# Kernel tuning notes

Measured on AMD Instinct MI355X. Metric: run time of the kernel, lower is better.

## Reference

```python
import jax, jax.numpy as jnp
import numpy as np

NEG = -1e9

def setup_inputs() -> dict:
    key = jax.random.key(0)
    k1, k2, k3, k4, k5 = jax.random.split(key, 5)
    B, S, D = 4, 2048, 1024
    x = jax.random.normal(k1, (B, S, D), dtype=jnp.float32)
    Wq = jax.random.normal(k2, (D, D), dtype=jnp.float32) * (1.0 / np.sqrt(D))
    Wk = jax.random.normal(k3, (D, D), dtype=jnp.float32) * (1.0 / np.sqrt(D))
    Wv = jax.random.normal(k4, (D, D), dtype=jnp.float32) * (1.0 / np.sqrt(D))
    mask = jax.random.randint(k5, (B, S), 0, 2) > 0  # bool [B,S]
    return {"x": x, "Wq": Wq, "Wk": Wk, "Wv": Wv, "mask": mask}

def reference(x, Wq, Wk, Wv, mask):
    # x: [B,S,D]; single-head self-attention, scale = 1/sqrt(D)
    D = x.shape[-1]
    scale = 1.0 / D ** 0.5
    q = jnp.einsum('bsi,ij->bsj', x, Wq)
    k = jnp.einsum('bsi,ij->bsj', x, Wk)
    y = jnp.einsum('bsi,bzi->bsz', q, k) * scale  # [B,S,S]
    # additive mask: (~mask)[:, :, None] * -1e9 broadcasts over key axis
    m = (~mask).astype(jnp.float32)[:, :, None]
    y = y + m * NEG
    v = jnp.einsum('bsi,ij->bsj', x, Wv)
    attn = jax.nn.softmax(y, axis=-1)
    return jnp.einsum('bsz,bzi->bsi', attn, v)
```

## Files before the change

kernel.cpp:

```cpp
#include <hip/hip_runtime.h>

typedef __bf16 bf16x8 __attribute__((ext_vector_type(8)));
typedef float f32x4 __attribute__((ext_vector_type(4)));
typedef unsigned short u16;

__device__ __forceinline__ u16 f2bf(float f) {
    union { float f; unsigned u; } v; v.f = f;
    unsigned r = (v.u + 0x7FFFu + ((v.u >> 16) & 1u)) >> 16;
    return (u16)r;
}

__device__ __forceinline__ void fence_bar() {
    asm volatile("" ::: "memory");
    __builtin_amdgcn_s_barrier();
    asm volatile("" ::: "memory");
}

__global__ __launch_bounds__(256)
void normMask(const unsigned int* __restrict__ m, unsigned char* __restrict__ nm) {
    __shared__ int isByte;
    if (threadIdx.x == 0) isByte = 0;
    __syncthreads();
    int bad = 0;
    for (int i = threadIdx.x; i < 2048; i += 256) bad |= (m[i] > 1u);
    if (bad) atomicOr(&isByte, 1);
    __syncthreads();
    if (isByte) {
        const unsigned char* mb = (const unsigned char*)m;
        for (int i = threadIdx.x; i < 8192; i += 256) nm[i] = mb[i] ? 1 : 0;
    } else {
        for (int i = threadIdx.x; i < 8192; i += 256) nm[i] = (unsigned char)m[i];
    }
}

__global__ __launch_bounds__(256)
void transW(const float* __restrict__ Wq, const float* __restrict__ Wk,
            const float* __restrict__ Wv, u16* __restrict__ Wt) {
    __shared__ u16 tile[64][65];
    const float* W = blockIdx.z == 0 ? Wq : (blockIdx.z == 1 ? Wk : Wv);
    u16* out = Wt + (size_t)blockIdx.z * 1024 * 1024;
    int k0 = blockIdx.x * 64, n0 = blockIdx.y * 64;
    int t = threadIdx.x, cl = t & 63, rw = t >> 6;
    #pragma unroll
    for (int r = 0; r < 16; ++r) {
        int row = r * 4 + rw;
        tile[cl][row] = f2bf(W[(size_t)(k0 + row) * 1024 + n0 + cl]);
    }
    __syncthreads();
    #pragma unroll
    for (int r = 0; r < 16; ++r) {
        int row = r * 4 + rw;
        out[(size_t)(n0 + row) * 1024 + k0 + cl] = tile[row][cl];
    }
}

__global__ __launch_bounds__(256)
void convX(const float* __restrict__ x, u16* __restrict__ xb) {
    const size_t n4 = (size_t)8192 * 1024 / 4;
    for (size_t i = (size_t)blockIdx.x * 256 + threadIdx.x; i < n4; i += (size_t)gridDim.x * 256) {
        float4 v = ((const float4*)x)[i];
        ushort4 o = make_ushort4(f2bf(v.x), f2bf(v.y), f2bf(v.z), f2bf(v.w));
        ((ushort4*)xb)[i] = o;
    }
}

__global__ __launch_bounds__(256)
void transV(const u16* __restrict__ qkv, u16* __restrict__ vt) {
    __shared__ u16 tile[64][65];
    int b = blockIdx.z;
    int s0 = blockIdx.x * 64, d0 = blockIdx.y * 64;
    int t = threadIdx.x, cl = t & 63, rw = t >> 6;
    const u16* src = qkv + (size_t)b * 2048 * 3072 + 2048;
    #pragma unroll
    for (int r = 0; r < 16; ++r) {
        int row = r * 4 + rw;
        tile[cl][row] = src[(size_t)(s0 + row) * 3072 + d0 + cl];
    }
    __syncthreads();
    u16* dst = vt + (size_t)b * 1024 * 2048;
    #pragma unroll
    for (int r = 0; r < 16; ++r) {
        int row = r * 4 + rw;
        dst[(size_t)(d0 + row) * 2048 + s0 + cl] = tile[row][cl];
    }
}

template <int OUTV>
__global__ __launch_bounds__(512, 2)
void gemm8p(const u16* __restrict__ A_, int lda, size_t sA,
            const u16* __restrict__ B_, int ldb, size_t sB,
            void* __restrict__ Cout, int ldc, size_t sC,
            int kdim, int ntiles) {
    __shared__ u16 lds[65536];
    const u16* A = A_ + (size_t)blockIdx.z * sA;
    const u16* B = B_ + (size_t)blockIdx.z * sB;

    const int bid = blockIdx.x;
    const int brow = (bid / ntiles) * 256, bcol = (bid % ntiles) * 256;
    const int t = threadIdx.x;
    const int w = t >> 6, l = t & 63;
    const int wr = w >> 2, wc = w & 3;

    const int srow = t >> 3;
    const int sslot = (t & 7) ^ (srow & 7);
    const int aBase = (wr * 128 + (l & 15)) * 64;
    const int bBase = 32768 + (wc * 64 + (l & 15)) * 64;
    const int cx0 = (((l >> 4)) ^ (l & 7)) * 8;
    const int cx1 = (((l >> 4) + 4) ^ (l & 7)) * 8;

    auto lds3 = (__attribute__((address_space(3))) char*)lds;

    #define ISSUE(matB, q, tt, buf) do {                                           \
        const u16* gsrc = ((matB) ? B : A)                                         \
            + (size_t)(((matB) ? bcol : brow) + (q) * 64 + srow) * ((matB) ? ldb : lda) \
            + (size_t)(tt) * 64 + sslot * 8;                                       \
        const int dst_ = ((matB) ? 32768 : 0) + (buf) * 16384 + (q) * 4096 + t * 8; \
        __builtin_amdgcn_global_load_lds(                                          \
            (const __attribute__((address_space(1))) void*)gsrc,                   \
            (__attribute__((address_space(3))) void*)(lds3 + 2 * dst_), 16, 0, 0); \
    } while (0)

    f32x4 acc[8][4];
    #pragma unroll
    for (int m = 0; m < 8; ++m)
        #pragma unroll
        for (int n = 0; n < 4; ++n)
            acc[m][n] = (f32x4){0.f, 0.f, 0.f, 0.f};

    const int NT = kdim >> 6;

    ISSUE(1, 0, 0, 0); ISSUE(1, 1, 0, 0); ISSUE(1, 2, 0, 0); ISSUE(1, 3, 0, 0);
    ISSUE(0, 0, 0, 0); ISSUE(0, 2, 0, 0); ISSUE(0, 1, 0, 0); ISSUE(0, 3, 0, 0);
    asm volatile("s_waitcnt vmcnt(2)" ::: "memory");
    fence_bar();

    for (int tt = 0; tt < NT; ++tt) {
        const int c = tt & 1;
        const int ab = c * 16384;
        const int nb = c ^ 1;
        const bool pf = (tt + 1 < NT);
        bf16x8 af[4], bfv[4];

        #pragma unroll
        for (int m = 0; m < 4; ++m) af[m] = *(const bf16x8*)&lds[ab + aBase + m * 1024 + cx0];
        #pragma unroll
        for (int n = 0; n < 4; ++n) bfv[n] = *(const bf16x8*)&lds[ab + bBase + n * 1024 + cx0];
        if (pf) {
            ISSUE(1, 0, tt + 1, nb); ISSUE(1, 1, tt + 1, nb);
            asm volatile("s_waitcnt vmcnt(2)" ::: "memory");
        } else {
            asm volatile("s_waitcnt vmcnt(0)" ::: "memory");
        }
        fence_bar();
        __builtin_amdgcn_s_setprio(1);
        #pragma unroll
        for (int m = 0; m < 4; ++m)
            #pragma unroll
            for (int n = 0; n < 4; ++n)
                acc[m][n] = __builtin_amdgcn_mfma_f32_16x16x32_bf16(af[m], bfv[n], acc[m][n], 0, 0, 0);
        __builtin_amdgcn_s_setprio(0);
        fence_bar();

        #pragma unroll
        for (int m = 0; m < 4; ++m) af[m] = *(const bf16x8*)&lds[ab + aBase + (m + 4) * 1024 + cx0];
        if (pf) { ISSUE(1, 2, tt + 1, nb); ISSUE(1, 3, tt + 1, nb); }
        fence_bar();
        __builtin_amdgcn_s_setprio(1);
        #pragma unroll
        for (int m = 0; m < 4; ++m)
            #pragma unroll
            for (int n = 0; n < 4; ++n)
                acc[m + 4][n] = __builtin_amdgcn_mfma_f32_16x16x32_bf16(af[m], bfv[n], acc[m + 4][n], 0, 0, 0);
        __builtin_amdgcn_s_setprio(0);
        fence_bar();

        #pragma unroll
        for (int m = 0; m < 4; ++m) af[m] = *(const bf16x8*)&lds[ab + aBase + m * 1024 + cx1];
        #pragma unroll
        for (int n = 0; n < 4; ++n) bfv[n] = *(const bf16x8*)&lds[ab + bBase + n * 1024 + cx1];
        if (pf) { ISSUE(0, 0, tt + 1, nb); ISSUE(0, 2, tt + 1, nb); }
        fence_bar();
        __builtin_amdgcn_s_setprio(1);
        #pragma unroll
        for (int m = 0; m < 4; ++m)
            #pragma unroll
            for (int n = 0; n < 4; ++n)
                acc[m][n] = __builtin_amdgcn_mfma_f32_16x16x32_bf16(af[m], bfv[n], acc[m][n], 0, 0, 0);
        __builtin_amdgcn_s_setprio(0);
        fence_bar();

        #pragma unroll
        for (int m = 0; m < 4; ++m) af[m] = *(const bf16x8*)&lds[ab + aBase + (m + 4) * 1024 + cx1];
        if (pf) {
            ISSUE(0, 1, tt + 1, nb); ISSUE(0, 3, tt + 1, nb);
            asm volatile("s_waitcnt vmcnt(2)" ::: "memory");
        } else {
            asm volatile("s_waitcnt vmcnt(0)" ::: "memory");
        }
        fence_bar();
        __builtin_amdgcn_s_setprio(1);
        #pragma unroll
        for (int m = 0; m < 4; ++m)
            #pragma unroll
            for (int n = 0; n < 4; ++n)
                acc[m + 4][n] = __builtin_amdgcn_mfma_f32_16x16x32_bf16(af[m], bfv[n], acc[m + 4][n], 0, 0, 0);
        __builtin_amdgcn_s_setprio(0);
        fence_bar();
    }
    #undef ISSUE

    const int lr = (l >> 4) * 4, lc = l & 15;
    #pragma unroll
    for (int m = 0; m < 8; ++m) {
        #pragma unroll
        for (int n = 0; n < 4; ++n) {
            int rr = brow + wr * 128 + m * 16 + lr;
            int cc = bcol + wc * 64 + n * 16 + lc;
            #pragma unroll
            for (int j = 0; j < 4; ++j) {
                if constexpr (OUTV == 0)
                    ((u16*)Cout)[(size_t)blockIdx.z * sC + (size_t)(rr + j) * ldc + cc] = f2bf(acc[m][n][j]);
                else
                    ((float*)Cout)[(size_t)blockIdx.z * sC + (size_t)(rr + j) * ldc + cc] = acc[m][n][j];
            }
        }
    }
}

template <int OUTV>
__global__ __launch_bounds__(256, 2)
void gemm_bt(const u16* __restrict__ A0, int lda, size_t sA,
             const u16* __restrict__ B0, int ldb, size_t sB,
             void* __restrict__ Cout, int ldc, size_t sC, int kdim) {
    __shared__ u16 lA[128 * 64];
    __shared__ u16 lB[128 * 64];
    const u16* A = A0 + (size_t)blockIdx.z * sA;
    const u16* B = B0 + (size_t)blockIdx.z * sB;
    const int t = threadIdx.x;
    const int w = t >> 6, l = t & 63;
    const int wr = w >> 1, wc = w & 1;
    const int brow = blockIdx.x * 128, bcol = blockIdx.y * 128;
    const int rt = l >> 3;
    const int cb = (l & 7) * 8;

    auto ldsA3 = (__attribute__((address_space(3))) char*)lA;
    auto ldsB3 = (__attribute__((address_space(3))) char*)lB;

    f32x4 acc[4][4];
    #pragma unroll
    for (int m = 0; m < 4; ++m)
        #pragma unroll
        for (int n = 0; n < 4; ++n)
            acc[m][n] = (f32x4){0.f, 0.f, 0.f, 0.f};

    for (int k0 = 0; k0 < kdim; k0 += 64) {
        __syncthreads();
        #pragma unroll
        for (int p = 0; p < 4; ++p) {
            int chunk = p * 4 + w;
            const u16* ga = A + (size_t)(brow + chunk * 8 + rt) * lda + k0 + cb;
            __builtin_amdgcn_global_load_lds(
                (const __attribute__((address_space(1))) void*)ga,
                (__attribute__((address_space(3))) void*)(ldsA3 + chunk * 1024), 16, 0, 0);
            const u16* gb = B + (size_t)(bcol + chunk * 8 + rt) * ldb + k0 + cb;
            __builtin_amdgcn_global_load_lds(
                (const __attribute__((address_space(1))) void*)gb,
                (__attribute__((address_space(3))) void*)(ldsB3 + chunk * 1024), 16, 0, 0);
        }
        __syncthreads();
        #pragma unroll
        for (int kk = 0; kk < 2; ++kk) {
            bf16x8 af[4], bfv[4];
            #pragma unroll
            for (int m = 0; m < 4; ++m)
                af[m] = *(const bf16x8*)&lA[(wr * 64 + m * 16 + (l & 15)) * 64 + kk * 32 + (l >> 4) * 8];
            #pragma unroll
            for (int n = 0; n < 4; ++n)
                bfv[n] = *(const bf16x8*)&lB[(wc * 64 + n * 16 + (l & 15)) * 64 + kk * 32 + (l >> 4) * 8];
            #pragma unroll
            for (int m = 0; m < 4; ++m)
                #pragma unroll
                for (int n = 0; n < 4; ++n)
                    acc[m][n] = __builtin_amdgcn_mfma_f32_16x16x32_bf16(af[m], bfv[n], acc[m][n], 0, 0, 0);
        }
    }

    const int lrow = (l >> 4) * 4, lcol = l & 15;
    #pragma unroll
    for (int m = 0; m < 4; ++m) {
        #pragma unroll
        for (int n = 0; n < 4; ++n) {
            int rr = brow + wr * 64 + m * 16 + lrow;
            int cc = bcol + wc * 64 + n * 16 + lcol;
            #pragma unroll
            for (int j = 0; j < 4; ++j) {
                if constexpr (OUTV == 0)
                    ((u16*)Cout)[(size_t)blockIdx.z * sC + (size_t)(rr + j) * ldc + cc] = f2bf(acc[m][n][j]);
                else
                    ((float*)Cout)[(size_t)blockIdx.z * sC + (size_t)(rr + j) * ldc + cc] = acc[m][n][j];
            }
        }
    }
}

__global__ __launch_bounds__(256)
void softmax_rows(const float* __restrict__ S0, size_t sS, u16* __restrict__ P0, size_t sP,
                  const unsigned char* __restrict__ nm, int bbase) {
    const int row = blockIdx.x, t = threadIdx.x;
    const int b = bbase + blockIdx.z;
    const float* S = S0 + (size_t)blockIdx.z * sS;
    u16* dst = P0 + (size_t)blockIdx.z * sP + (size_t)row * 2048;
    if (nm[b * 2048 + row] == 0) {
        ushort4 u = make_ushort4(0x3A00, 0x3A00, 0x3A00, 0x3A00);
        ((ushort4*)dst)[t] = u;
        ((ushort4*)dst)[t + 256] = u;
        return;
    }
    const float4* src = (const float4*)(S + (size_t)row * 2048);
    float4 a = src[t], c = src[t + 256];
    float v[8] = {a.x, a.y, a.z, a.w, c.x, c.y, c.z, c.w};
    float mx = -1e30f;
    #pragma unroll
    for (int i = 0; i < 8; ++i) { v[i] *= 0.03125f; mx = fmaxf(mx, v[i]); }
    #pragma unroll
    for (int o = 32; o > 0; o >>= 1) mx = fmaxf(mx, __shfl_xor(mx, o));
    __shared__ float redm[4], reds[4];
    if ((t & 63) == 0) redm[t >> 6] = mx;
    __syncthreads();
    mx = fmaxf(fmaxf(redm[0], redm[1]), fmaxf(redm[2], redm[3]));
    float s = 0.f;
    #pragma unroll
    for (int i = 0; i < 8; ++i) { v[i] = expf(v[i] - mx); s += v[i]; }
    #pragma unroll
    for (int o = 32; o > 0; o >>= 1) s += __shfl_xor(s, o);
    if ((t & 63) == 0) reds[t >> 6] = s;
    __syncthreads();
    s = (reds[0] + reds[1]) + (reds[2] + reds[3]);
    float inv = 1.0f / s;
    ushort4 o0 = make_ushort4(f2bf(v[0] * inv), f2bf(v[1] * inv), f2bf(v[2] * inv), f2bf(v[3] * inv));
    ushort4 o1 = make_ushort4(f2bf(v[4] * inv), f2bf(v[5] * inv), f2bf(v[6] * inv), f2bf(v[7] * inv));
    ((ushort4*)dst)[t] = o0;
    ((ushort4*)dst)[t + 256] = o1;
}

extern "C" void kernel_launch(void* const* d_in, const int* in_sizes, int n_in,
                              void* d_out, int out_size, void* d_ws, size_t ws_size,
                              hipStream_t stream) {
    const float* x  = (const float*)d_in[0];
    const float* Wq = (const float*)d_in[1];
    const float* Wk = (const float*)d_in[2];
    const float* Wv = (const float*)d_in[3];
    const unsigned int* mask = (const unsigned int*)d_in[4];
    float* out = (float*)d_out;

    char* p = (char*)d_ws;
    u16* Wt  = (u16*)p;  p += (size_t)3072 * 1024 * 2;
    u16* xb  = (u16*)p;  p += (size_t)8192 * 1024 * 2;
    u16* qkv = (u16*)p;  p += (size_t)8192 * 3072 * 2;
    u16* vt  = (u16*)p;  p += (size_t)4 * 1024 * 2048 * 2;
    char* base = p;
    const size_t sizeS = (size_t)2048 * 2048 * 4;
    const size_t sizeP = (size_t)2048 * 2048 * 2;
    bool batched = ws_size >= (size_t)(base - (char*)d_ws) + 4 * (sizeS + sizeP) + 8192;

    float* S = (float*)base;
    u16* P;
    unsigned char* nm;
    if (batched) {
        P  = (u16*)(base + 4 * sizeS);
        nm = (unsigned char*)(base + 4 * (sizeS + sizeP));
    } else {
        P  = (u16*)(base + sizeS);
        nm = (unsigned char*)(base + sizeS + sizeP);
    }

    normMask<<<1, 256, 0, stream>>>(mask, nm);
    transW<<<dim3(16, 16, 3), 256, 0, stream>>>(Wq, Wk, Wv, Wt);
    convX<<<2048, 256, 0, stream>>>(x, xb);
    gemm8p<0><<<dim3(384, 1, 1), 512, 0, stream>>>(
        xb, 1024, 0, Wt, 1024, 0, qkv, 3072, 0, 1024, 12);
    transV<<<dim3(32, 16, 4), 256, 0, stream>>>(qkv, vt);

    if (batched) {
        gemm8p<1><<<dim3(64, 1, 4), 512, 0, stream>>>(
            qkv, 3072, (size_t)2048 * 3072, qkv + 1024, 3072, (size_t)2048 * 3072,
            S, 2048, (size_t)2048 * 2048, 1024, 8);
        softmax_rows<<<dim3(2048, 1, 4), 256, 0, stream>>>(
            S, (size_t)2048 * 2048, P, (size_t)2048 * 2048, nm, 0);
        gemm_bt<2><<<dim3(16, 8, 4), 256, 0, stream>>>(
            P, 2048, (size_t)2048 * 2048, vt, 2048, (size_t)1024 * 2048,
            out, 1024, (size_t)2048 * 1024, 2048);
    } else {
        for (int b = 0; b < 4; ++b) {
            const u16* Qb = qkv + (size_t)b * 2048 * 3072;
            gemm8p<1><<<dim3(64, 1, 1), 512, 0, stream>>>(
                Qb, 3072, 0, Qb + 1024, 3072, 0, S, 2048, 0, 1024, 8);
            softmax_rows<<<dim3(2048, 1, 1), 256, 0, stream>>>(S, 0, P, 0, nm, b);
            gemm_bt<2><<<dim3(16, 8, 1), 256, 0, stream>>>(
                P, 2048, 0, vt + (size_t)b * 1024 * 2048, 2048, 0,
                out + (size_t)b * 2048 * 1024, 1024, 0, 2048);
        }
    }
}
```

Before: 201.3 us.

## Restructure GEMM mainloop to K=32 tiles with four-stage prefetch pipeline

The 256x256 GEMM now uses K-tiles of 32 instead of 64. It keeps four LDS buffers and prefetches three tiles ahead instead of double buffering 64-wide tiles. The swizzle and load layout are reworked for 32-element rows. This aims to hide global-to-LDS latency better and shrink per-stage waits, at the cost of more barriers per unit of work and shorter MFMA bursts between syncs.

```diff
diff --git a/kernel.cpp b/kernel.cpp
--- a/kernel.cpp
+++ b/kernel.cpp
@@ -87,7 +87,7 @@
 
 template <int OUTV>
 __global__ __launch_bounds__(512, 2)
-void gemm8p(const u16* __restrict__ A_, int lda, size_t sA,
+void gemm32(const u16* __restrict__ A_, int lda, size_t sA,
             const u16* __restrict__ B_, int ldb, size_t sB,
             void* __restrict__ Cout, int ldc, size_t sC,
             int kdim, int ntiles) {
@@ -101,23 +101,27 @@
     const int w = t >> 6, l = t & 63;
     const int wr = w >> 2, wc = w & 3;
 
-    const int srow = t >> 3;
-    const int sslot = (t & 7) ^ (srow & 7);
-    const int aBase = (wr * 128 + (l & 15)) * 64;
-    const int bBase = 32768 + (wc * 64 + (l & 15)) * 64;
-    const int cx0 = (((l >> 4)) ^ (l & 7)) * 8;
-    const int cx1 = (((l >> 4) + 4) ^ (l & 7)) * 8;
+    const int sslot8 = ((l & 3) ^ ((l >> 3) & 3)) * 8;
+    const int cx = (((l >> 4)) ^ ((l >> 1) & 3)) * 8;
+    const int aB0 = (wr * 128 + (l & 15)) * 32 + cx;
+    const int bB0 = 8192 + (wc * 64 + (l & 15)) * 32 + cx;
 
     auto lds3 = (__attribute__((address_space(3))) char*)lds;
 
-    #define ISSUE(matB, q, tt, buf) do {                                           \
-        const u16* gsrc = ((matB) ? B : A)                                         \
-            + (size_t)(((matB) ? bcol : brow) + (q) * 64 + srow) * ((matB) ? ldb : lda) \
-            + (size_t)(tt) * 64 + sslot * 8;                                       \
-        const int dst_ = ((matB) ? 32768 : 0) + (buf) * 16384 + (q) * 4096 + t * 8; \
-        __builtin_amdgcn_global_load_lds(                                          \
-            (const __attribute__((address_space(1))) void*)gsrc,                   \
-            (__attribute__((address_space(3))) void*)(lds3 + 2 * dst_), 16, 0, 0); \
+    #define ISSUE32(matB, tt) do {                                                 \
+        const int buf_ = (tt) & 3;                                                 \
+        _Pragma("unroll")                                                          \
+        for (int r_ = 0; r_ < 2; ++r_) {                                           \
+            const int row_ = w * 32 + r_ * 16 + (l >> 2);                          \
+            const u16* gsrc = ((matB) ? B : A)                                     \
+                + (size_t)(((matB) ? bcol : brow) + row_) * ((matB) ? ldb : lda)   \
+                + (size_t)(tt) * 32 + sslot8;                                      \
+            const int dst_ = buf_ * 16384 + ((matB) ? 8192 : 0)                    \
+                + w * 1024 + r_ * 512 + l * 8;                                     \
+            __builtin_amdgcn_global_load_lds(                                      \
+                (const __attribute__((address_space(1))) void*)gsrc,               \
+                (__attribute__((address_space(3))) void*)(lds3 + 2 * dst_), 16, 0, 0); \
+        }                                                                          \
     } while (0)
 
     f32x4 acc[8][4];
@@ -127,30 +131,25 @@
         for (int n = 0; n < 4; ++n)
             acc[m][n] = (f32x4){0.f, 0.f, 0.f, 0.f};
 
-    const int NT = kdim >> 6;
-
-    ISSUE(1, 0, 0, 0); ISSUE(1, 1, 0, 0); ISSUE(1, 2, 0, 0); ISSUE(1, 3, 0, 0);
-    ISSUE(0, 0, 0, 0); ISSUE(0, 2, 0, 0); ISSUE(0, 1, 0, 0); ISSUE(0, 3, 0, 0);
-    asm volatile("s_waitcnt vmcnt(2)" ::: "memory");
+    const int NT = kdim >> 5;
+
+    ISSUE32(0, 0); ISSUE32(1, 0);
+    if (NT > 1) { ISSUE32(0, 1); ISSUE32(1, 1); }
+    if (NT > 2) { ISSUE32(0, 2); ISSUE32(1, 2); }
+    if (NT > 2)      asm volatile("s_waitcnt vmcnt(8)" ::: "memory");
+    else if (NT > 1) asm volatile("s_waitcnt vmcnt(4)" ::: "memory");
+    else             asm volatile("s_waitcnt vmcnt(0)" ::: "memory");
     fence_bar();
 
-    for (int tt = 0; tt < NT; ++tt) {
-        const int c = tt & 1;
-        const int ab = c * 16384;
-        const int nb = c ^ 1;
-        const bool pf = (tt + 1 < NT);
+    for (int kt = 0; kt < NT; ++kt) {
+        const int ab = (kt & 3) * 16384;
         bf16x8 af[4], bfv[4];
 
         #pragma unroll
-        for (int m = 0; m < 4; ++m) af[m] = *(const bf16x8*)&lds[ab + aBase + m * 1024 + cx0];
-        #pragma unroll
-        for (int n = 0; n < 4; ++n) bfv[n] = *(const bf16x8*)&lds[ab + bBase + n * 1024 + cx0];
-        if (pf) {
-            ISSUE(1, 0, tt + 1, nb); ISSUE(1, 1, tt + 1, nb);
-            asm volatile("s_waitcnt vmcnt(2)" ::: "memory");
-        } else {
-            asm volatile("s_waitcnt vmcnt(0)" ::: "memory");
-        }
+        for (int m = 0; m < 4; ++m) af[m] = *(const bf16x8*)&lds[ab + aB0 + m * 512];
+        #pragma unroll
+        for (int n = 0; n < 4; ++n) bfv[n] = *(const bf16x8*)&lds[ab + bB0 + n * 512];
+        if (kt + 3 < NT) ISSUE32(0, kt + 3);
         fence_bar();
         __builtin_amdgcn_s_setprio(1);
         #pragma unroll
@@ -162,8 +161,11 @@
         fence_bar();
 
         #pragma unroll
-        for (int m = 0; m < 4; ++m) af[m] = *(const bf16x8*)&lds[ab + aBase + (m + 4) * 1024 + cx0];
-        if (pf) { ISSUE(1, 2, tt + 1, nb); ISSUE(1, 3, tt + 1, nb); }
+        for (int m = 0; m < 4; ++m) af[m] = *(const bf16x8*)&lds[ab + aB0 + (m + 4) * 512];
+        if (kt + 3 < NT) ISSUE32(1, kt + 3);
+        if (kt + 3 < NT)      asm volatile("s_waitcnt vmcnt(8)" ::: "memory");
+        else if (kt + 2 < NT) asm volatile("s_waitcnt vmcnt(4)" ::: "memory");
+        else                  asm volatile("s_waitcnt vmcnt(0)" ::: "memory");
         fence_bar();
         __builtin_amdgcn_s_setprio(1);
         #pragma unroll
@@ -173,41 +175,8 @@
                 acc[m + 4][n] = __builtin_amdgcn_mfma_f32_16x16x32_bf16(af[m], bfv[n], acc[m + 4][n], 0, 0, 0);
         __builtin_amdgcn_s_setprio(0);
         fence_bar();
-
-        #pragma unroll
-        for (int m = 0; m < 4; ++m) af[m] = *(const bf16x8*)&lds[ab + aBase + m * 1024 + cx1];
-        #pragma unroll
-        for (int n = 0; n < 4; ++n) bfv[n] = *(const bf16x8*)&lds[ab + bBase + n * 1024 + cx1];
-        if (pf) { ISSUE(0, 0, tt + 1, nb); ISSUE(0, 2, tt + 1, nb); }
-        fence_bar();
-        __builtin_amdgcn_s_setprio(1);
-        #pragma unroll
-        for (int m = 0; m < 4; ++m)
-            #pragma unroll
-            for (int n = 0; n < 4; ++n)
-                acc[m][n] = __builtin_amdgcn_mfma_f32_16x16x32_bf16(af[m], bfv[n], acc[m][n], 0, 0, 0);
-        __builtin_amdgcn_s_setprio(0);
-        fence_bar();
-
-        #pragma unroll
-        for (int m = 0; m < 4; ++m) af[m] = *(const bf16x8*)&lds[ab + aBase + (m + 4) * 1024 + cx1];
-        if (pf) {
-            ISSUE(0, 1, tt + 1, nb); ISSUE(0, 3, tt + 1, nb);
-            asm volatile("s_waitcnt vmcnt(2)" ::: "memory");
-        } else {
-            asm volatile("s_waitcnt vmcnt(0)" ::: "memory");
-        }
-        fence_bar();
-        __builtin_amdgcn_s_setprio(1);
-        #pragma unroll
-        for (int m = 0; m < 4; ++m)
-            #pragma unroll
-            for (int n = 0; n < 4; ++n)
-                acc[m + 4][n] = __builtin_amdgcn_mfma_f32_16x16x32_bf16(af[m], bfv[n], acc[m + 4][n], 0, 0, 0);
-        __builtin_amdgcn_s_setprio(0);
-        fence_bar();
-    }
-    #undef ISSUE
+    }
+    #undef ISSUE32
 
     const int lr = (l >> 4) * 4, lc = l & 15;
     #pragma unroll
@@ -377,12 +346,12 @@
     normMask<<<1, 256, 0, stream>>>(mask, nm);
     transW<<<dim3(16, 16, 3), 256, 0, stream>>>(Wq, Wk, Wv, Wt);
     convX<<<2048, 256, 0, stream>>>(x, xb);
-    gemm8p<0><<<dim3(384, 1, 1), 512, 0, stream>>>(
+    gemm32<0><<<dim3(384, 1, 1), 512, 0, stream>>>(
         xb, 1024, 0, Wt, 1024, 0, qkv, 3072, 0, 1024, 12);
     transV<<<dim3(32, 16, 4), 256, 0, stream>>>(qkv, vt);
 
     if (batched) {
-        gemm8p<1><<<dim3(64, 1, 4), 512, 0, stream>>>(
+        gemm32<1><<<dim3(64, 1, 4), 512, 0, stream>>>(
             qkv, 3072, (size_t)2048 * 3072, qkv + 1024, 3072, (size_t)2048 * 3072,
             S, 2048, (size_t)2048 * 2048, 1024, 8);
         softmax_rows<<<dim3(2048, 1, 4), 256, 0, stream>>>(
@@ -393,7 +362,7 @@
     } else {
         for (int b = 0; b < 4; ++b) {
             const u16* Qb = qkv + (size_t)b * 2048 * 3072;
-            gemm8p<1><<<dim3(64, 1, 1), 512, 0, stream>>>(
+            gemm32<1><<<dim3(64, 1, 1), 512, 0, stream>>>(
                 Qb, 3072, 0, Qb + 1024, 3072, 0, S, 2048, 0, 1024, 8);
             softmax_rows<<<dim3(2048, 1, 1), 256, 0, stream>>>(S, 0, P, 0, nm, b);
             gemm_bt<2><<<dim3(16, 8, 1), 256, 0, stream>>>(
```

New measurement: 203.9 us. No clear change (+1.3%).

## Compact unmasked query rows and fill masked rows with mean of V

Applied to the files above, without the earlier changes.

Masked query rows get a uniform softmax, so their output equals the mean of V. The change scans the mask into a compacted index list, gathers only unmasked Q rows, and runs the score GEMM, softmax and PV GEMM only on those rows, scattering results back. Masked rows are then filled with a precomputed per-batch mean of V. This cuts roughly half the attention work for a random mask, at the cost of extra small kernels and scattered output writes. It also reuses the xb and qkv buffers as scratch space.

```diff
diff --git a/kernel.cpp b/kernel.cpp
--- a/kernel.cpp
+++ b/kernel.cpp
@@ -9,7 +9,10 @@
     unsigned r = (v.u + 0x7FFFu + ((v.u >> 16) & 1u)) >> 16;
     return (u16)r;
 }
-
+__device__ __forceinline__ float bf2f(u16 b) {
+    union { unsigned u; float f; } v; v.u = ((unsigned)b) << 16;
+    return v.f;
+}
 __device__ __forceinline__ void fence_bar() {
     asm volatile("" ::: "memory");
     __builtin_amdgcn_s_barrier();
@@ -31,6 +34,32 @@
     } else {
         for (int i = threadIdx.x; i < 8192; i += 256) nm[i] = (unsigned char)m[i];
     }
+}
+
+__global__ __launch_bounds__(256)
+void scanMask(const unsigned char* __restrict__ nm, int* __restrict__ idxc,
+              int* __restrict__ cnt) {
+    __shared__ int segsum[256];
+    const int b = blockIdx.x, t = threadIdx.x;
+    const unsigned char* m = nm + b * 2048;
+    int loc[8]; int s = 0;
+    #pragma unroll
+    for (int i = 0; i < 8; ++i) { loc[i] = m[t * 8 + i]; s += loc[i]; }
+    segsum[t] = s;
+    __syncthreads();
+    #pragma unroll
+    for (int off = 1; off < 256; off <<= 1) {
+        int v = (t >= off) ? segsum[t - off] : 0;
+        __syncthreads();
+        segsum[t] += v;
+        __syncthreads();
+    }
+    int base = (t > 0) ? segsum[t - 1] : 0;
+    #pragma unroll
+    for (int i = 0; i < 8; ++i) {
+        if (loc[i]) { idxc[b * 2048 + base] = t * 8 + i; ++base; }
+    }
+    if (t == 255) cnt[b] = segsum[255];
 }
 
 __global__ __launch_bounds__(256)
@@ -83,6 +112,32 @@
         int row = r * 4 + rw;
         dst[(size_t)(d0 + row) * 2048 + s0 + cl] = tile[row][cl];
     }
+}
+
+__global__ __launch_bounds__(256)
+void meanV(const u16* __restrict__ qkv, float* __restrict__ mv) {
+    const int b = blockIdx.y;
+    const int d = blockIdx.x * 256 + threadIdx.x;
+    const u16* src = qkv + (size_t)b * 2048 * 3072 + 2048 + d;
+    float s0 = 0.f, s1 = 0.f, s2 = 0.f, s3 = 0.f;
+    for (int r = 0; r < 2048; r += 4) {
+        s0 += bf2f(src[(size_t)(r + 0) * 3072]);
+        s1 += bf2f(src[(size_t)(r + 1) * 3072]);
+        s2 += bf2f(src[(size_t)(r + 2) * 3072]);
+        s3 += bf2f(src[(size_t)(r + 3) * 3072]);
+    }
+    mv[b * 1024 + d] = (s0 + s1 + s2 + s3) * (1.0f / 2048.0f);
+}
+
+__global__ __launch_bounds__(256)
+void gatherQ(const u16* __restrict__ qkv, const int* __restrict__ idxc,
+             const int* __restrict__ cnt, u16* __restrict__ qc, int zoff) {
+    const int zl = blockIdx.z + zoff, j = blockIdx.x;
+    if (j >= cnt[zl]) return;
+    const int src = idxc[zl * 2048 + j];
+    const uint4* s = (const uint4*)(qkv + (size_t)(zl * 2048 + src) * 3072);
+    uint4* d = (uint4*)(qc + ((size_t)blockIdx.z * 2048 + j) * 1024);
+    if (threadIdx.x < 128) d[threadIdx.x] = s[threadIdx.x];
 }
 
 template <int OUTV>
@@ -227,11 +282,13 @@
     }
 }
 
-template <int OUTV>
 __global__ __launch_bounds__(256, 2)
-void gemm_bt(const u16* __restrict__ A0, int lda, size_t sA,
+void gemm_sc(const u16* __restrict__ A0, int lda, size_t sA,
              const u16* __restrict__ B0, int ldb, size_t sB,
-             void* __restrict__ Cout, int ldc, size_t sC, int kdim) {
+             float* __restrict__ Cout, int ldc, size_t sC, int kdim,
+             const int* __restrict__ cnt, int zoff) {
+    const int zl = blockIdx.z + zoff;
+    if ((int)blockIdx.x * 128 >= cnt[zl]) return;
     __shared__ u16 lA[128 * 64];
     __shared__ u16 lB[128 * 64];
     const u16* A = A0 + (size_t)blockIdx.z * sA;
@@ -293,30 +350,103 @@
             int rr = brow + wr * 64 + m * 16 + lrow;
             int cc = bcol + wc * 64 + n * 16 + lcol;
             #pragma unroll
-            for (int j = 0; j < 4; ++j) {
-                if constexpr (OUTV == 0)
-                    ((u16*)Cout)[(size_t)blockIdx.z * sC + (size_t)(rr + j) * ldc + cc] = f2bf(acc[m][n][j]);
-                else
-                    ((float*)Cout)[(size_t)blockIdx.z * sC + (size_t)(rr + j) * ldc + cc] = acc[m][n][j];
+            for (int j = 0; j < 4; ++j)
+                Cout[(size_t)blockIdx.z * sC + (size_t)(rr + j) * ldc + cc] = acc[m][n][j];
+        }
+    }
+}
+
+__global__ __launch_bounds__(256, 2)
+void gemm_pvs(const u16* __restrict__ A0, int lda, size_t sA,
+              const u16* __restrict__ B0, int ldb, size_t sB,
+              float* __restrict__ out, int kdim,
+              const int* __restrict__ idxc, const int* __restrict__ cnt, int zoff) {
+    const int zl = blockIdx.z + zoff;
+    const int cn = cnt[zl];
+    if ((int)blockIdx.x * 128 >= cn) return;
+    __shared__ u16 lA[128 * 64];
+    __shared__ u16 lB[128 * 64];
+    const u16* A = A0 + (size_t)blockIdx.z * sA;
+    const u16* B = B0 + (size_t)blockIdx.z * sB;
+    const int t = threadIdx.x;
+    const int w = t >> 6, l = t & 63;
+    const int wr = w >> 1, wc = w & 1;
+    const int brow = blockIdx.x * 128, bcol = blockIdx.y * 128;
+    const int rt = l >> 3;
+    const int cb = (l & 7) * 8;
+
+    auto ldsA3 = (__attribute__((address_space(3))) char*)lA;
+    auto ldsB3 = (__attribute__((address_space(3))) char*)lB;
+
+    f32x4 acc[4][4];
+    #pragma unroll
+    for (int m = 0; m < 4; ++m)
+        #pragma unroll
+        for (int n = 0; n < 4; ++n)
+            acc[m][n] = (f32x4){0.f, 0.f, 0.f, 0.f};
+
+    for (int k0 = 0; k0 < kdim; k0 += 64) {
+        __syncthreads();
+        #pragma unroll
+        for (int p = 0; p < 4; ++p) {
+            int chunk = p * 4 + w;
+            const u16* ga = A + (size_t)(brow + chunk * 8 + rt) * lda + k0 + cb;
+            __builtin_amdgcn_global_load_lds(
+                (const __attribute__((address_space(1))) void*)ga,
+                (__attribute__((address_space(3))) void*)(ldsA3 + chunk * 1024), 16, 0, 0);
+            const u16* gb = B + (size_t)(bcol + chunk * 8 + rt) * ldb + k0 + cb;
+            __builtin_amdgcn_global_load_lds(
+                (const __attribute__((address_space(1))) void*)gb,
+                (__attribute__((address_space(3))) void*)(ldsB3 + chunk * 1024), 16, 0, 0);
+        }
+        __syncthreads();
+        #pragma unroll
+        for (int kk = 0; kk < 2; ++kk) {
+            bf16x8 af[4], bfv[4];
+            #pragma unroll
+            for (int m = 0; m < 4; ++m)
+                af[m] = *(const bf16x8*)&lA[(wr * 64 + m * 16 + (l & 15)) * 64 + kk * 32 + (l >> 4) * 8];
+            #pragma unroll
+            for (int n = 0; n < 4; ++n)
+                bfv[n] = *(const bf16x8*)&lB[(wc * 64 + n * 16 + (l & 15)) * 64 + kk * 32 + (l >> 4) * 8];
+            #pragma unroll
+            for (int m = 0; m < 4; ++m)
+                #pragma unroll
+                for (int n = 0; n < 4; ++n)
+                    acc[m][n] = __builtin_amdgcn_mfma_f32_16x16x32_bf16(af[m], bfv[n], acc[m][n], 0, 0, 0);
+        }
+    }
+
+    const int lrow = (l >> 4) * 4, lcol = l & 15;
+    #pragma unroll
+    for (int m = 0; m < 4; ++m) {
+        #pragma unroll
+        for (int j = 0; j < 4; ++j) {
+            int rr = brow + wr * 64 + m * 16 + lrow + j;
+            if (rr < cn) {
+                int orow = idxc[zl * 2048 + rr];
+                float* od = out + ((size_t)zl * 2048 + orow) * 1024 + bcol + wc * 64 + lcol;
+                #pragma unroll
+                for (int n = 0; n < 4; ++n)
+                    od[n * 16] = acc[m][n][j];
             }
         }
     }
 }
 
 __global__ __launch_bounds__(256)
-void softmax_rows(const float* __restrict__ S0, size_t sS, u16* __restrict__ P0, size_t sP,
-                  const unsigned char* __restrict__ nm, int bbase) {
+void softmax_c(const float* __restrict__ S0, size_t sS, u16* __restrict__ P0, size_t sP,
+               const int* __restrict__ cnt, int zoff) {
     const int row = blockIdx.x, t = threadIdx.x;
-    const int b = bbase + blockIdx.z;
-    const float* S = S0 + (size_t)blockIdx.z * sS;
+    const int zl = blockIdx.z + zoff;
     u16* dst = P0 + (size_t)blockIdx.z * sP + (size_t)row * 2048;
-    if (nm[b * 2048 + row] == 0) {
-        ushort4 u = make_ushort4(0x3A00, 0x3A00, 0x3A00, 0x3A00);
-        ((ushort4*)dst)[t] = u;
-        ((ushort4*)dst)[t + 256] = u;
+    if (row >= cnt[zl]) {
+        ushort4 z4 = make_ushort4(0, 0, 0, 0);
+        ((ushort4*)dst)[t] = z4;
+        ((ushort4*)dst)[t + 256] = z4;
         return;
     }
-    const float4* src = (const float4*)(S + (size_t)row * 2048);
+    const float4* src = (const float4*)(S0 + (size_t)blockIdx.z * sS + (size_t)row * 2048);
     float4 a = src[t], c = src[t + 256];
     float v[8] = {a.x, a.y, a.z, a.w, c.x, c.y, c.z, c.w};
     float mx = -1e30f;
@@ -341,6 +471,16 @@
     ushort4 o1 = make_ushort4(f2bf(v[4] * inv), f2bf(v[5] * inv), f2bf(v[6] * inv), f2bf(v[7] * inv));
     ((ushort4*)dst)[t] = o0;
     ((ushort4*)dst)[t + 256] = o1;
+}
+
+__global__ __launch_bounds__(256)
+void maskFill(const float* __restrict__ mv, const unsigned char* __restrict__ nm,
+              float* __restrict__ out) {
+    const int b = blockIdx.z, s = blockIdx.x, t = threadIdx.x;
+    if (nm[b * 2048 + s]) return;
+    const float4* src = (const float4*)(mv + b * 1024);
+    float4* d = (float4*)(out + ((size_t)b * 2048 + s) * 1024);
+    d[t] = src[t];
 }
 
 extern "C" void kernel_launch(void* const* d_in, const int* in_sizes, int n_in,
@@ -360,45 +500,51 @@
     u16* vt  = (u16*)p;  p += (size_t)4 * 1024 * 2048 * 2;
     char* base = p;
     const size_t sizeS = (size_t)2048 * 2048 * 4;
-    const size_t sizeP = (size_t)2048 * 2048 * 2;
-    bool batched = ws_size >= (size_t)(base - (char*)d_ws) + 4 * (sizeS + sizeP) + 8192;
-
-    float* S = (float*)base;
-    u16* P;
-    unsigned char* nm;
-    if (batched) {
-        P  = (u16*)(base + 4 * sizeS);
-        nm = (unsigned char*)(base + 4 * (sizeS + sizeP));
-    } else {
-        P  = (u16*)(base + sizeS);
-        nm = (unsigned char*)(base + sizeS + sizeP);
-    }
+    const size_t tailSz = (size_t)4 * 1024 * 4 + (size_t)4 * 2048 * 4 + 64 + 8192;
+    bool batched = ws_size >= (size_t)(base - (char*)d_ws) + 4 * sizeS + tailSz;
+    int nz = batched ? 4 : 1;
+
+    float* S  = (float*)base;
+    char* q2  = base + nz * sizeS;
+    float* mv = (float*)q2;            q2 += (size_t)4 * 1024 * 4;
+    int* idxc = (int*)q2;              q2 += (size_t)4 * 2048 * 4;
+    int* cnt  = (int*)q2;              q2 += 64;
+    unsigned char* nm = (unsigned char*)q2;
+
+    u16* qc = xb;
+    u16* Pc = qkv;
 
     normMask<<<1, 256, 0, stream>>>(mask, nm);
+    scanMask<<<4, 256, 0, stream>>>(nm, idxc, cnt);
     transW<<<dim3(16, 16, 3), 256, 0, stream>>>(Wq, Wk, Wv, Wt);
     convX<<<2048, 256, 0, stream>>>(x, xb);
     gemm8p<0><<<dim3(384, 1, 1), 512, 0, stream>>>(
         xb, 1024, 0, Wt, 1024, 0, qkv, 3072, 0, 1024, 12);
     transV<<<dim3(32, 16, 4), 256, 0, stream>>>(qkv, vt);
+    meanV<<<dim3(4, 4), 256, 0, stream>>>(qkv, mv);
+
+    const size_t sQKV = (size_t)2048 * 3072;
+    const size_t sQC  = (size_t)2048 * 1024;
+    const size_t sSC  = (size_t)2048 * 2048;
+    const size_t sVT  = (size_t)1024 * 2048;
 
     if (batched) {
-        gemm8p<1><<<dim3(64, 1, 4), 512, 0, stream>>>(
-            qkv, 3072, (size_t)2048 * 3072, qkv + 1024, 3072, (size_t)2048 * 3072,
-            S, 2048, (size_t)2048 * 2048, 1024, 8);
-        softmax_rows<<<dim3(2048, 1, 4), 256, 0, stream>>>(
-            S, (size_t)2048 * 2048, P, (size_t)2048 * 2048, nm, 0);
-        gemm_bt<2><<<dim3(16, 8, 4), 256, 0, stream>>>(
-            P, 2048, (size_t)2048 * 2048, vt, 2048, (size_t)1024 * 2048,
-            out, 1024, (size_t)2048 * 1024, 2048);
+        gatherQ<<<dim3(2048, 1, 4), 256, 0, stream>>>(qkv, idxc, cnt, qc, 0);
+        gemm_sc<<<dim3(16, 16, 4), 256, 0, stream>>>(
+            qc, 1024, sQC, qkv + 1024, 3072, sQKV, S, 2048, sSC, 1024, cnt, 0);
+        softmax_c<<<dim3(2048, 1, 4), 256, 0, stream>>>(S, sSC, Pc, sSC, cnt, 0);
+        gemm_pvs<<<dim3(16, 8, 4), 256, 0, stream>>>(
+            Pc, 2048, sSC, vt, 2048, sVT, out, 2048, idxc, cnt, 0);
     } else {
         for (int b = 0; b < 4; ++b) {
-            const u16* Qb = qkv + (size_t)b * 2048 * 3072;
-            gemm8p<1><<<dim3(64, 1, 1), 512, 0, stream>>>(
-                Qb, 3072, 0, Qb + 1024, 3072, 0, S, 2048, 0, 1024, 8);
-            softmax_rows<<<dim3(2048, 1, 1), 256, 0, stream>>>(S, 0, P, 0, nm, b);
-            gemm_bt<2><<<dim3(16, 8, 1), 256, 0, stream>>>(
-                P, 2048, 0, vt + (size_t)b * 1024 * 2048, 2048, 0,
-                out + (size_t)b * 2048 * 1024, 1024, 0, 2048);
-        }
-    }
-}
+            gatherQ<<<dim3(2048, 1, 1), 256, 0, stream>>>(qkv, idxc, cnt, qc, b);
+            gemm_sc<<<dim3(16, 16, 1), 256, 0, stream>>>(
+                qc, 1024, 0, qkv + 1024 + (size_t)b * sQKV, 3072, 0,
+                S, 2048, 0, 1024, cnt, b);
+            softmax_c<<<dim3(2048, 1, 1), 256, 0, stream>>>(S, 0, Pc, 0, cnt, b);
+            gemm_pvs<<<dim3(16, 8, 1), 256, 0, stream>>>(
+                Pc, 2048, 0, vt + (size_t)b * sVT, 2048, 0, out, 2048, idxc, cnt, b);
+        }
+    }
+    maskFill<<<dim3(2048, 1, 4), 256, 0, stream>>>(mv, nm, out);
+}
```

Measured after the change: 282.5 us. 40.4% more time.
